# Kernel tuning notes

Hardware: AMD Instinct MI355X
Metric: run time of the kernel (lower is better)

The kernel has to match this reference:

```python
import jax, jax.numpy as jnp
import numpy as np

B, N, C, H = 4, 2048, 768, 12
D = C // H  # head_dim = 64

def setup_inputs() -> dict:
    key = jax.random.key(0)
    ks = jax.random.split(key, 6)
    s = 0.02
    return {
        "img_tokens": jax.random.normal(ks[0], (B, N, C), jnp.float32),
        "ln_gamma": jnp.ones((C,), jnp.float32),
        "ln_beta": jnp.zeros((C,), jnp.float32),
        "w_qkv": jax.random.normal(ks[1], (C, 3 * C), jnp.float32) * s,
        "w_out": jax.random.normal(ks[2], (C, C), jnp.float32) * s,
        "b_out": jnp.zeros((C,), jnp.float32),
    }

def reference(img_tokens, ln_gamma, ln_beta, w_qkv, w_out, b_out):
    x = img_tokens
    # LayerNorm over channel dim
    mu = jnp.mean(x, axis=-1, keepdims=True)
    var = jnp.var(x, axis=-1, keepdims=True)
    xn = (x - mu) * jax.lax.rsqrt(var + 1e-5) * ln_gamma + ln_beta
    qkv = xn @ w_qkv                      # [B, N, 3C]
    q, k, v = jnp.split(qkv, 3, axis=-1)
    def heads(t):                          # [B, N, C] -> [B, H, N, D]
        return t.reshape(B, N, H, D).transpose(0, 2, 1, 3)
    q, k, v = heads(q), heads(k), heads(v)
    scale = 1.0 / np.sqrt(D).astype(np.float32)
    scores = jnp.einsum('bhnd,bhmd->bhnm', q, k) * scale  # [B, H, N, N]
    attn = jax.nn.softmax(scores, axis=-1)
    out = jnp.einsum('bhnm,bhmd->bhnd', attn, v)          # [B, H, N, D]
    out = out.transpose(0, 2, 1, 3).reshape(B, N, C)
    out = out @ w_out + b_out
    return out + img_tokens
```

## Files before the change

kernel.cpp:

```cpp
#include <hip/hip_runtime.h>


typedef __bf16 bf16x8 __attribute__((ext_vector_type(8)));
typedef float  f32x4  __attribute__((ext_vector_type(4)));
typedef unsigned int u32x4 __attribute__((ext_vector_type(4)));

#define MFMA16(a,b,c) __builtin_amdgcn_mfma_f32_16x16x32_bf16((a),(b),(c),0,0,0)

__device__ inline f32x4 zero4() { f32x4 z = {0.f,0.f,0.f,0.f}; return z; }

__device__ inline void gll16(const __bf16* g, __bf16* l) {
  __builtin_amdgcn_global_load_lds((const __attribute__((address_space(1))) unsigned int*)g,
                                   (__attribute__((address_space(3))) unsigned int*)l,
                                   16, 0, 0);
}

__device__ inline unsigned cvt_pk_bf16(float lo, float hi) {
  unsigned r;
  asm("v_cvt_pk_bf16_f32 %0, %1, %2" : "=v"(r) : "v"(lo), "v"(hi));
  return r;
}
__device__ inline void permlane32_swap(unsigned &a, unsigned &b) {
  asm("v_permlane32_swap_b32 %0, %1" : "+v"(a), "+v"(b));
}
__device__ inline void permlane16_swap(unsigned &a, unsigned &b) {
  asm("v_permlane16_swap_b32 %0, %1" : "+v"(a), "+v"(b));
}

__global__ __launch_bounds__(256) void ln_kernel(const float* __restrict__ x,
                                                 const float* __restrict__ g,
                                                 const float* __restrict__ bt,
                                                 __bf16* __restrict__ xn) {
  const int row = blockIdx.x;
  const int tid = threadIdx.x;
  const float* xr = x + (size_t)row * 768;
  float v[3]; float s = 0.f, ss = 0.f;
  #pragma unroll
  for (int i = 0; i < 3; ++i) { float f = xr[tid + 256*i]; v[i] = f; s += f; ss += f*f; }
  #pragma unroll
  for (int m = 32; m >= 1; m >>= 1) { s += __shfl_xor(s, m, 64); ss += __shfl_xor(ss, m, 64); }
  __shared__ float red[8];
  const int wave = tid >> 6;
  if ((tid & 63) == 0) { red[wave] = s; red[4 + wave] = ss; }
  __syncthreads();
  s  = red[0] + red[1] + red[2] + red[3];
  ss = red[4] + red[5] + red[6] + red[7];
  const float mu  = s * (1.f/768.f);
  const float var = ss * (1.f/768.f) - mu*mu;
  const float inv = rsqrtf(var + 1e-5f);
  __bf16* xo = xn + (size_t)row * 768;
  #pragma unroll
  for (int i = 0; i < 3; ++i) {
    const int c0 = tid + 256*i;
    xo[c0] = (__bf16)((v[i] - mu) * inv * g[c0] + bt[c0]);
  }
}

__global__ __launch_bounds__(256) void transpose_kernel(const float* __restrict__ in,
                                                        __bf16* __restrict__ out,
                                                        int R, int C) {
  __shared__ float t[32][33];
  const int tx = threadIdx.x & 31, ty = threadIdx.x >> 5;
  const int c0 = blockIdx.x * 32, r0 = blockIdx.y * 32;
  #pragma unroll
  for (int p = 0; p < 4; ++p) t[ty + 8*p][tx] = in[(size_t)(r0 + ty + 8*p) * C + c0 + tx];
  __syncthreads();
  #pragma unroll
  for (int p = 0; p < 4; ++p) out[(size_t)(c0 + ty + 8*p) * R + r0 + tx] = (__bf16)t[tx][ty + 8*p];
}

template<int KDIM>
__device__ inline void gemm_mainloop(const __bf16* __restrict__ A, const __bf16* __restrict__ BT,
                                     int bm, int bn, int wave, int lane,
                                     f32x4 acc[4][4], __bf16* Asm, __bf16* Bsm) {
  const int wm = wave >> 1, wn = wave & 1;
  const int lr = lane & 15, lk = lane >> 4;
  for (int k0 = 0; k0 < KDIM; k0 += 64) {
    #pragma unroll
    for (int s2 = 0; s2 < 4; ++s2) {
      const int st = wave * 4 + s2;
      const int rb = st >> 1, kh = st & 1;
      gll16(A  + (size_t)(bm + rb*16 + lr) * KDIM + k0 + kh*32 + lk*8, Asm + st*512);
      gll16(BT + (size_t)(bn + rb*16 + lr) * KDIM + k0 + kh*32 + lk*8, Bsm + st*512);
    }
    __builtin_amdgcn_s_waitcnt(0);
    __syncthreads();
    #pragma unroll
    for (int ks = 0; ks < 2; ++ks) {
      bf16x8 a[4], b[4];
      #pragma unroll
      for (int mt = 0; mt < 4; ++mt) a[mt] = *(const bf16x8*)(Asm + ((wm*4+mt)*2+ks)*512 + lane*8);
      #pragma unroll
      for (int nt = 0; nt < 4; ++nt) b[nt] = *(const bf16x8*)(Bsm + ((wn*4+nt)*2+ks)*512 + lane*8);
      #pragma unroll
      for (int mt = 0; mt < 4; ++mt)
        #pragma unroll
        for (int nt = 0; nt < 4; ++nt)
          acc[mt][nt] = MFMA16(a[mt], b[nt], acc[mt][nt]);
    }
    __syncthreads();
  }
}

__global__ __launch_bounds__(256) void gemm_qkv_kernel(const __bf16* __restrict__ A,
                                                       const __bf16* __restrict__ BT,
                                                       __bf16* __restrict__ q,
                                                       __bf16* __restrict__ k,
                                                       __bf16* __restrict__ vt) {
  __shared__ __align__(16) __bf16 smem[2*8192];
  __bf16* Asm = smem;
  __bf16* Bsm = smem + 8192;
  const int lane = threadIdx.x & 63, wave = threadIdx.x >> 6;
  const int bm = blockIdx.y * 128, bn = blockIdx.x * 128;
  f32x4 acc[4][4];
  #pragma unroll
  for (int i = 0; i < 4; ++i)
    #pragma unroll
    for (int j = 0; j < 4; ++j) acc[i][j] = zero4();
  gemm_mainloop<768>(A, BT, bm, bn, wave, lane, acc, Asm, Bsm);
  const int wm = wave >> 1, wn = wave & 1;
  const int quad = lane >> 4, c = lane & 15;
  if (bn < 1536) {
    const float qscale = 0.125f * 1.44269504088896f;
    #pragma unroll
    for (int mt = 0; mt < 4; ++mt)
      #pragma unroll
      for (int nt = 0; nt < 4; ++nt) {
        const int col = bn + wn*64 + nt*16 + c;
        const int which = col >= 768 ? 1 : 0;
        const int within = col - which*768;
        const int h = within >> 6, d = within & 63;
        #pragma unroll
        for (int r = 0; r < 4; ++r) {
          const int row = bm + wm*64 + mt*16 + quad*4 + r;
          const int b = row >> 11, n = row & 2047;
          const float vv = acc[mt][nt][r];
          const size_t idx = ((size_t)(b*12 + h) * 2048 + n) * 64 + d;
          if (which == 0) q[idx] = (__bf16)(vv * qscale);
          else            k[idx] = (__bf16)vv;
        }
      }
  } else {
    __syncthreads();
    #pragma unroll
    for (int mt = 0; mt < 4; ++mt)
      #pragma unroll
      for (int nt = 0; nt < 4; ++nt) {
        const int lcol = wn*64 + nt*16 + c;
        #pragma unroll
        for (int r = 0; r < 4; ++r) {
          const int lrow = wm*64 + mt*16 + quad*4 + r;
          smem[lrow*66 + lcol] = (__bf16)acc[mt][nt][r];
        }
      }
    __syncthreads();
    const int b = bm >> 11, n0 = bm & 2047;
    const int vo = bn - 1536;
    const int n = threadIdx.x & 127;
    const int csel = threadIdx.x >> 7;
    #pragma unroll
    for (int pass = 0; pass < 64; ++pass) {
      const int lc = pass*2 + csel;
      const int gcol = vo + lc;
      const int h = gcol >> 6, d = gcol & 63;
      vt[((size_t)(b*12 + h)*64 + d)*2048 + n0 + n] = smem[n*66 + lc];
    }
  }
}

__global__ __launch_bounds__(256) void gemm_out_kernel(const __bf16* __restrict__ A,
                                                       const __bf16* __restrict__ BT,
                                                       const float* __restrict__ bias,
                                                       const float* __restrict__ resid,
                                                       float* __restrict__ out) {
  __shared__ __align__(16) __bf16 Asm[16*512];
  __shared__ __align__(16) __bf16 Bsm[16*512];
  const int lane = threadIdx.x & 63, wave = threadIdx.x >> 6;
  const int bm = blockIdx.y * 128, bn = blockIdx.x * 128;
  f32x4 acc[4][4];
  #pragma unroll
  for (int i = 0; i < 4; ++i)
    #pragma unroll
    for (int j = 0; j < 4; ++j) acc[i][j] = zero4();
  gemm_mainloop<768>(A, BT, bm, bn, wave, lane, acc, Asm, Bsm);
  const int wm = wave >> 1, wn = wave & 1;
  const int quad = lane >> 4, c = lane & 15;
  #pragma unroll
  for (int mt = 0; mt < 4; ++mt)
    #pragma unroll
    for (int nt = 0; nt < 4; ++nt) {
      const int col = bn + wn*64 + nt*16 + c;
      #pragma unroll
      for (int r = 0; r < 4; ++r) {
        const int row = bm + wm*64 + mt*16 + quad*4 + r;
        out[(size_t)row*768 + col] = acc[mt][nt][r] + bias[col] + resid[(size_t)row*768 + col];
      }
    }
}

__global__ __launch_bounds__(256) void attn_kernel(const __bf16* __restrict__ q,
                                                   const __bf16* __restrict__ k,
                                                   const __bf16* __restrict__ vt,
                                                   __bf16* __restrict__ o) {
  const int xcd = blockIdx.x & 7, i = blockIdx.x >> 3;
  const int bh = xcd * 6 + (i >> 4);
  const int qt = i & 15;
  const int lane = threadIdx.x & 63, wave = threadIdx.x >> 6;
  const int c = lane & 15, quad = lane >> 4;
  const int lr = lane & 15, lk = lane >> 4;
  const int q0 = qt*128 + wave*32;

  const __bf16* qb = q  + ((size_t)bh*2048 + q0) * 64;
  const __bf16* kb = k  + (size_t)bh * 2048 * 64;
  const __bf16* vb = vt + (size_t)bh * 64 * 2048;

  __shared__ __align__(16) __bf16 Ksm[2][4096];
  __shared__ __align__(16) __bf16 Vsm[2][4096];

  bf16x8 aq[2][2];
  #pragma unroll
  for (int rg = 0; rg < 2; ++rg) {
    aq[rg][0] = *(const bf16x8*)(qb + (size_t)(rg*16 + c)*64 + quad*8);
    aq[rg][1] = *(const bf16x8*)(qb + (size_t)(rg*16 + c)*64 + 32 + quad*8);
  }

  float cl[2];
  f32x4 od[2][4];
  #pragma unroll
  for (int rg = 0; rg < 2; ++rg) {
    cl[rg] = 0.f;
    #pragma unroll
    for (int r = 0; r < 4; ++r) od[rg][r] = zero4();
  }

  auto stage = [&](int it) {
    const int kt = it * 64;
    __bf16* Ks = Ksm[it & 1];
    __bf16* Vs = Vsm[it & 1];
    gll16(kb + (size_t)(kt + wave*16 + lr) * 64 + lk*8,        Ks + (wave*2+0)*512);
    gll16(kb + (size_t)(kt + wave*16 + lr) * 64 + 32 + lk*8,   Ks + (wave*2+1)*512);
    gll16(vb + (size_t)(wave*16 + lr) * 2048 + kt + lk*8,      Vs + (wave*2+0)*512);
    gll16(vb + (size_t)(wave*16 + lr) * 2048 + kt + 32 + lk*8, Vs + (wave*2+1)*512);
  };

  stage(0);
  stage(1);

  for (int it = 0; it < 32; ++it) {
    const __bf16* Ks = Ksm[it & 1];
    const __bf16* Vs = Vsm[it & 1];
    if (it < 31) asm volatile("s_waitcnt vmcnt(4)" ::: "memory");
    else         asm volatile("s_waitcnt vmcnt(0)" ::: "memory");
    asm volatile("s_barrier" ::: "memory");
    #pragma unroll
    for (int ch = 0; ch < 2; ++ch) {
      unsigned pk[2][2][2];
      #pragma unroll
      for (int t2 = 0; t2 < 2; ++t2) {
        const int t = ch*2 + t2;
        const bf16x8 ka0 = *(const bf16x8*)(Ks + (t*2+0)*512 + lane*8);
        const bf16x8 ka1 = *(const bf16x8*)(Ks + (t*2+1)*512 + lane*8);
        #pragma unroll
        for (int rg = 0; rg < 2; ++rg) {
          f32x4 z = zero4();
          z = MFMA16(ka0, aq[rg][0], z);
          z = MFMA16(ka1, aq[rg][1], z);
          const float p0 = __builtin_amdgcn_exp2f(z[0]);
          const float p1 = __builtin_amdgcn_exp2f(z[1]);
          const float p2 = __builtin_amdgcn_exp2f(z[2]);
          const float p3 = __builtin_amdgcn_exp2f(z[3]);
          cl[rg] += (p0 + p1) + (p2 + p3);
          pk[rg][t2][0] = cvt_pk_bf16(p0, p1);
          pk[rg][t2][1] = cvt_pk_bf16(p2, p3);
        }
      }
      bf16x8 pa[2];
      #pragma unroll
      for (int rg = 0; rg < 2; ++rg) {
        unsigned s0 = pk[rg][0][0], s2 = pk[rg][1][0];
        permlane32_swap(s0, s2);
        permlane16_swap(s0, s2);
        unsigned s1 = pk[rg][0][1], s3 = pk[rg][1][1];
        permlane32_swap(s1, s3);
        permlane16_swap(s1, s3);
        u32x4 w4; w4.x = s0; w4.y = s1; w4.z = s2; w4.w = s3;
        pa[rg] = __builtin_bit_cast(bf16x8, w4);
      }
      #pragma unroll
      for (int dt = 0; dt < 4; ++dt) {
        const bf16x8 bv = *(const bf16x8*)(Vs + (dt*2+ch)*512 + lane*8);
        od[0][dt] = MFMA16(pa[0], bv, od[0][dt]);
        od[1][dt] = MFMA16(pa[1], bv, od[1][dt]);
      }
    }
    asm volatile("s_barrier" ::: "memory");
    if (it + 2 < 32) stage(it + 2);
  }
  const int b = bh / 12, h = bh % 12;
  #pragma unroll
  for (int rg = 0; rg < 2; ++rg) {
    float s = cl[rg];
    s += __shfl_xor(s, 16, 64);
    s += __shfl_xor(s, 32, 64);
    float rl[4];
    #pragma unroll
    for (int r = 0; r < 4; ++r) rl[r] = 1.f / __shfl(s, quad*4 + r, 64);
    #pragma unroll
    for (int dt = 0; dt < 4; ++dt)
      #pragma unroll
      for (int r = 0; r < 4; ++r) {
        const int n = q0 + rg*16 + quad*4 + r;
        const int col = h*64 + dt*16 + c;
        o[((size_t)b*2048 + n)*768 + col] = (__bf16)(od[rg][dt][r] * rl[r]);
      }
  }
}

extern "C" void kernel_launch(void* const* d_in, const int* in_sizes, int n_in,
                              void* d_out, int out_size, void* d_ws, size_t ws_size,
                              hipStream_t stream) {
  const float* img   = (const float*)d_in[0];
  const float* gamma = (const float*)d_in[1];
  const float* beta  = (const float*)d_in[2];
  const float* wqkv  = (const float*)d_in[3];
  const float* wout  = (const float*)d_in[4];
  const float* bout  = (const float*)d_in[5];
  float* out = (float*)d_out;

  __bf16* ws = (__bf16*)d_ws;
  size_t off = 0;
  __bf16* xn    = ws + off; off += (size_t)8192*768;
  __bf16* wqkvT = ws + off; off += (size_t)2304*768;
  __bf16* woutT = ws + off; off += (size_t)768*768;
  __bf16* qs    = ws + off; off += (size_t)48*2048*64;
  __bf16* ks    = ws + off; off += (size_t)48*2048*64;
  __bf16* vts   = ws + off; off += (size_t)48*64*2048;
  __bf16* os    = ws + off; off += (size_t)8192*768;

  ln_kernel<<<8192, 256, 0, stream>>>(img, gamma, beta, xn);
  transpose_kernel<<<dim3(72, 24), 256, 0, stream>>>(wqkv, wqkvT, 768, 2304);
  transpose_kernel<<<dim3(24, 24), 256, 0, stream>>>(wout, woutT, 768, 768);
  gemm_qkv_kernel<<<dim3(18, 64), 256, 0, stream>>>(xn, wqkvT, qs, ks, vts);
  attn_kernel<<<768, 256, 0, stream>>>(qs, ks, vts, os);
  gemm_out_kernel<<<dim3(6, 64), 256, 0, stream>>>(os, woutT, bout, img, out);
}
```

Before: 272.3 us.

## Split attention work across 8 waves with 16 query rows each, add MFMA priority

The attention kernel now launches 512 threads per block, so each of 8 waves handles 16 query rows instead of 4 waves handling 32. K/V tile staging is redistributed so each wave issues one load per tile, and the vmcnt wait is adjusted to match. s_setprio is raised around the MFMA sections so matrix ops take issue priority over the exp and permute work from other waves. This aims to increase latency hiding through more waves per CU and lower register pressure per wave, at the cost of each K/V fragment read from LDS being reused by only one row group instead of two.

```diff
diff --git a/kernel.cpp b/kernel.cpp
--- a/kernel.cpp
+++ b/kernel.cpp
@@ -198,17 +198,17 @@
     }
 }
 
-__global__ __launch_bounds__(256) void attn_kernel(const __bf16* __restrict__ q,
-                                                   const __bf16* __restrict__ k,
-                                                   const __bf16* __restrict__ vt,
-                                                   __bf16* __restrict__ o) {
+__global__ __launch_bounds__(512, 6) void attn_kernel(const __bf16* __restrict__ q,
+                                                      const __bf16* __restrict__ k,
+                                                      const __bf16* __restrict__ vt,
+                                                      __bf16* __restrict__ o) {
   const int xcd = blockIdx.x & 7, i = blockIdx.x >> 3;
   const int bh = xcd * 6 + (i >> 4);
   const int qt = i & 15;
   const int lane = threadIdx.x & 63, wave = threadIdx.x >> 6;
   const int c = lane & 15, quad = lane >> 4;
   const int lr = lane & 15, lk = lane >> 4;
-  const int q0 = qt*128 + wave*32;
+  const int q0 = qt*128 + wave*16;
 
   const __bf16* qb = q  + ((size_t)bh*2048 + q0) * 64;
   const __bf16* kb = k  + (size_t)bh * 2048 * 64;
@@ -217,30 +217,21 @@
   __shared__ __align__(16) __bf16 Ksm[2][4096];
   __shared__ __align__(16) __bf16 Vsm[2][4096];
 
-  bf16x8 aq[2][2];
-  #pragma unroll
-  for (int rg = 0; rg < 2; ++rg) {
-    aq[rg][0] = *(const bf16x8*)(qb + (size_t)(rg*16 + c)*64 + quad*8);
-    aq[rg][1] = *(const bf16x8*)(qb + (size_t)(rg*16 + c)*64 + 32 + quad*8);
-  }
-
-  float cl[2];
-  f32x4 od[2][4];
-  #pragma unroll
-  for (int rg = 0; rg < 2; ++rg) {
-    cl[rg] = 0.f;
-    #pragma unroll
-    for (int r = 0; r < 4; ++r) od[rg][r] = zero4();
-  }
+  bf16x8 aq[2];
+  aq[0] = *(const bf16x8*)(qb + (size_t)c*64 + quad*8);
+  aq[1] = *(const bf16x8*)(qb + (size_t)c*64 + 32 + quad*8);
+
+  float cl = 0.f;
+  f32x4 od[4];
+  #pragma unroll
+  for (int r = 0; r < 4; ++r) od[r] = zero4();
 
   auto stage = [&](int it) {
     const int kt = it * 64;
     __bf16* Ks = Ksm[it & 1];
     __bf16* Vs = Vsm[it & 1];
-    gll16(kb + (size_t)(kt + wave*16 + lr) * 64 + lk*8,        Ks + (wave*2+0)*512);
-    gll16(kb + (size_t)(kt + wave*16 + lr) * 64 + 32 + lk*8,   Ks + (wave*2+1)*512);
-    gll16(vb + (size_t)(wave*16 + lr) * 2048 + kt + lk*8,      Vs + (wave*2+0)*512);
-    gll16(vb + (size_t)(wave*16 + lr) * 2048 + kt + 32 + lk*8, Vs + (wave*2+1)*512);
+    gll16(kb + (size_t)(kt + (wave>>1)*16 + lr) * 64 + (wave&1)*32 + lk*8,  Ks + wave*512);
+    gll16(vb + (size_t)((wave>>1)*16 + lr) * 2048 + kt + (wave&1)*32 + lk*8, Vs + wave*512);
   };
 
   stage(0);
@@ -249,71 +240,64 @@
   for (int it = 0; it < 32; ++it) {
     const __bf16* Ks = Ksm[it & 1];
     const __bf16* Vs = Vsm[it & 1];
-    if (it < 31) asm volatile("s_waitcnt vmcnt(4)" ::: "memory");
+    if (it < 31) asm volatile("s_waitcnt vmcnt(2)" ::: "memory");
     else         asm volatile("s_waitcnt vmcnt(0)" ::: "memory");
     asm volatile("s_barrier" ::: "memory");
     #pragma unroll
     for (int ch = 0; ch < 2; ++ch) {
-      unsigned pk[2][2][2];
+      unsigned pk[2][2];
       #pragma unroll
       for (int t2 = 0; t2 < 2; ++t2) {
         const int t = ch*2 + t2;
         const bf16x8 ka0 = *(const bf16x8*)(Ks + (t*2+0)*512 + lane*8);
         const bf16x8 ka1 = *(const bf16x8*)(Ks + (t*2+1)*512 + lane*8);
-        #pragma unroll
-        for (int rg = 0; rg < 2; ++rg) {
-          f32x4 z = zero4();
-          z = MFMA16(ka0, aq[rg][0], z);
-          z = MFMA16(ka1, aq[rg][1], z);
-          const float p0 = __builtin_amdgcn_exp2f(z[0]);
-          const float p1 = __builtin_amdgcn_exp2f(z[1]);
-          const float p2 = __builtin_amdgcn_exp2f(z[2]);
-          const float p3 = __builtin_amdgcn_exp2f(z[3]);
-          cl[rg] += (p0 + p1) + (p2 + p3);
-          pk[rg][t2][0] = cvt_pk_bf16(p0, p1);
-          pk[rg][t2][1] = cvt_pk_bf16(p2, p3);
-        }
-      }
-      bf16x8 pa[2];
-      #pragma unroll
-      for (int rg = 0; rg < 2; ++rg) {
-        unsigned s0 = pk[rg][0][0], s2 = pk[rg][1][0];
-        permlane32_swap(s0, s2);
-        permlane16_swap(s0, s2);
-        unsigned s1 = pk[rg][0][1], s3 = pk[rg][1][1];
-        permlane32_swap(s1, s3);
-        permlane16_swap(s1, s3);
-        u32x4 w4; w4.x = s0; w4.y = s1; w4.z = s2; w4.w = s3;
-        pa[rg] = __builtin_bit_cast(bf16x8, w4);
-      }
+        f32x4 z = zero4();
+        __builtin_amdgcn_s_setprio(1);
+        z = MFMA16(ka0, aq[0], z);
+        z = MFMA16(ka1, aq[1], z);
+        __builtin_amdgcn_s_setprio(0);
+        const float p0 = __builtin_amdgcn_exp2f(z[0]);
+        const float p1 = __builtin_amdgcn_exp2f(z[1]);
+        const float p2 = __builtin_amdgcn_exp2f(z[2]);
+        const float p3 = __builtin_amdgcn_exp2f(z[3]);
+        cl += (p0 + p1) + (p2 + p3);
+        pk[t2][0] = cvt_pk_bf16(p0, p1);
+        pk[t2][1] = cvt_pk_bf16(p2, p3);
+      }
+      unsigned s0 = pk[0][0], s2 = pk[1][0];
+      permlane32_swap(s0, s2);
+      permlane16_swap(s0, s2);
+      unsigned s1 = pk[0][1], s3 = pk[1][1];
+      permlane32_swap(s1, s3);
+      permlane16_swap(s1, s3);
+      u32x4 w4; w4.x = s0; w4.y = s1; w4.z = s2; w4.w = s3;
+      const bf16x8 pa = __builtin_bit_cast(bf16x8, w4);
+      __builtin_amdgcn_s_setprio(1);
       #pragma unroll
       for (int dt = 0; dt < 4; ++dt) {
         const bf16x8 bv = *(const bf16x8*)(Vs + (dt*2+ch)*512 + lane*8);
-        od[0][dt] = MFMA16(pa[0], bv, od[0][dt]);
-        od[1][dt] = MFMA16(pa[1], bv, od[1][dt]);
-      }
+        od[dt] = MFMA16(pa, bv, od[dt]);
+      }
+      __builtin_amdgcn_s_setprio(0);
     }
     asm volatile("s_barrier" ::: "memory");
     if (it + 2 < 32) stage(it + 2);
   }
   const int b = bh / 12, h = bh % 12;
-  #pragma unroll
-  for (int rg = 0; rg < 2; ++rg) {
-    float s = cl[rg];
-    s += __shfl_xor(s, 16, 64);
-    s += __shfl_xor(s, 32, 64);
-    float rl[4];
-    #pragma unroll
-    for (int r = 0; r < 4; ++r) rl[r] = 1.f / __shfl(s, quad*4 + r, 64);
-    #pragma unroll
-    for (int dt = 0; dt < 4; ++dt)
-      #pragma unroll
-      for (int r = 0; r < 4; ++r) {
-        const int n = q0 + rg*16 + quad*4 + r;
-        const int col = h*64 + dt*16 + c;
-        o[((size_t)b*2048 + n)*768 + col] = (__bf16)(od[rg][dt][r] * rl[r]);
-      }
-  }
+  float s = cl;
+  s += __shfl_xor(s, 16, 64);
+  s += __shfl_xor(s, 32, 64);
+  float rl[4];
+  #pragma unroll
+  for (int r = 0; r < 4; ++r) rl[r] = 1.f / __shfl(s, quad*4 + r, 64);
+  #pragma unroll
+  for (int dt = 0; dt < 4; ++dt)
+    #pragma unroll
+    for (int r = 0; r < 4; ++r) {
+      const int n = q0 + quad*4 + r;
+      const int col = h*64 + dt*16 + c;
+      o[((size_t)b*2048 + n)*768 + col] = (__bf16)(od[dt][r] * rl[r]);
+    }
 }
 
 extern "C" void kernel_launch(void* const* d_in, const int* in_sizes, int n_in,
@@ -341,6 +325,6 @@
   transpose_kernel<<<dim3(72, 24), 256, 0, stream>>>(wqkv, wqkvT, 768, 2304);
   transpose_kernel<<<dim3(24, 24), 256, 0, stream>>>(wout, woutT, 768, 768);
   gemm_qkv_kernel<<<dim3(18, 64), 256, 0, stream>>>(xn, wqkvT, qs, ks, vts);
-  attn_kernel<<<768, 256, 0, stream>>>(qs, ks, vts, os);
+  attn_kernel<<<768, 512, 0, stream>>>(qs, ks, vts, os);
   gemm_out_kernel<<<dim3(6, 64), 256, 0, stream>>>(os, woutT, bout, img, out);
 }
```

Measured after the change: 254.8 us. -6.4%, faster.
